# Optimization experiments

Hardware: AMD Instinct MI355X
Metric: run time of the kernel (lower is better)

The kernel has to match this reference:

```python
import jax, jax.numpy as jnp
import numpy as np

B, T, C, H = 2, 2048, 1024, 16
D = C // H  # head_dim = 64


def setup_inputs() -> dict:
    key = jax.random.key(0)
    ks = jax.random.split(key, 5)
    s = 1.0 / np.sqrt(C)
    return {
        "x": jax.random.normal(ks[0], (B, T, C), jnp.float32),
        "Wq": jax.random.normal(ks[1], (C, C), jnp.float32) * s,
        "bq": jnp.zeros((C,), jnp.float32),
        "Wk": jax.random.normal(ks[2], (C, C), jnp.float32) * s,
        "bk": jnp.zeros((C,), jnp.float32),
        "Wv": jax.random.normal(ks[3], (C, C), jnp.float32) * s,
        "bv": jnp.zeros((C,), jnp.float32),
        "Wo": jax.random.normal(ks[4], (C, C), jnp.float32) * s,
        "bo": jnp.zeros((C,), jnp.float32),
    }


def reference(x, Wq, bq, Wk, bk, Wv, bv, Wo, bo):
    Bx, Tx, Cx = x.shape
    # torch Linear: y = x @ W.T + b
    q = (x @ Wq.T + bq).reshape(Bx, Tx, H, D).transpose(0, 2, 1, 3)  # [B,H,T,D]
    k = (x @ Wk.T + bk).reshape(Bx, Tx, H, D).transpose(0, 2, 1, 3)
    v = (x @ Wv.T + bv).reshape(Bx, Tx, H, D).transpose(0, 2, 1, 3)
    att = jnp.einsum("bhqd,bhkd->bhqk", q, k) / np.sqrt(D).astype(np.float32)
    mask = jnp.tril(jnp.ones((Tx, Tx), bool))  # causal mask [T,T]
    att = jnp.where(mask, att, -jnp.inf)
    att = jax.nn.softmax(att, axis=-1)
    out = jnp.einsum("bhqk,bhkd->bhqd", att, v)
    out = out.transpose(0, 2, 1, 3).reshape(Bx, Tx, Cx)
    return out @ Wo.T + bo
```

## Files before the change

kernel.cpp:

```cpp
#include <hip/hip_runtime.h>
#include <hip/hip_bf16.h>

#define B_ 2
#define T_ 2048
#define C_ 1024
#define H_ 16
#define D_ 64

typedef unsigned short u16;
typedef __bf16 bf16x8 __attribute__((ext_vector_type(8)));
typedef float floatx4 __attribute__((ext_vector_type(4)));

__device__ __forceinline__ float bf2f(u16 u) {
  union { unsigned int i; float f; } x; x.i = ((unsigned int)u) << 16; return x.f;
}
__device__ __forceinline__ u16 f2bf(float f) {
  union { float f; unsigned int i; } x; x.f = f;
  unsigned int r = x.i + 0x7fffu + ((x.i >> 16) & 1u);
  return (u16)(r >> 16);
}

__device__ __forceinline__ unsigned cvtpk(float lo, float hi) {
  unsigned r;
  asm("v_cvt_pk_bf16_f32 %0, %1, %2" : "=v"(r) : "v"(lo), "v"(hi));
  return r;
}

__device__ __forceinline__ void gld16(void* lds, const void* g) {
  __builtin_amdgcn_global_load_lds(
      (const __attribute__((address_space(1))) unsigned int*)g,
      (__attribute__((address_space(3))) unsigned int*)lds, 16, 0, 0);
}

#define NXF4 1048576
#define NWF4 262144

__global__ __launch_bounds__(256) void cvt_all(
    const float* __restrict__ x,  const float* __restrict__ Wq,
    const float* __restrict__ Wk, const float* __restrict__ Wv,
    const float* __restrict__ Wo, u16* __restrict__ dst_base)
{
  const int i = blockIdx.x * 256 + threadIdx.x;
  const float* src; size_t off;
  if (i < NXF4)               { src = x;  off = i; }
  else if (i < NXF4 + NWF4)   { src = Wq; off = i - NXF4; }
  else if (i < NXF4 + 2*NWF4) { src = Wk; off = i - (NXF4 + NWF4); }
  else if (i < NXF4 + 3*NWF4) { src = Wv; off = i - (NXF4 + 2*NWF4); }
  else                        { src = Wo; off = i - (NXF4 + 3*NWF4); }
  float4 f = ((const float4*)src)[off];
  ushort4 o;
  o.x = f2bf(f.x); o.y = f2bf(f.y); o.z = f2bf(f.z); o.w = f2bf(f.w);
  ((ushort4*)dst_base)[i] = o;
}

#define QSCALE 0.1803368801111f

#define MFMA16(MH, NH, BREG)                                                  \
  do {                                                                        \
    __builtin_amdgcn_s_setprio(1);                                            \
    _Pragma("unroll")                                                         \
    for (int f = 0; f < 4; ++f) {                                             \
      _Pragma("unroll")                                                       \
      for (int g = 0; g < 2; ++g) {                                           \
        acc[(MH)*4 + f][(NH)*2 + g] = __builtin_amdgcn_mfma_f32_16x16x32_bf16(\
            a[f][0], BREG[g][0], acc[(MH)*4 + f][(NH)*2 + g], 0, 0, 0);       \
        acc[(MH)*4 + f][(NH)*2 + g] = __builtin_amdgcn_mfma_f32_16x16x32_bf16(\
            a[f][1], BREG[g][1], acc[(MH)*4 + f][(NH)*2 + g], 0, 0, 0);       \
      }                                                                       \
    }                                                                         \
    __builtin_amdgcn_s_setprio(0);                                            \
  } while (0)

#define PBAR()                                                \
  do {                                                        \
    asm volatile("" ::: "memory");                            \
    __builtin_amdgcn_s_barrier();                             \
    asm volatile("s_waitcnt lgkmcnt(0)" ::: "memory");        \
  } while (0)

#define EBAR()                                                \
  do {                                                        \
    asm volatile("" ::: "memory");                            \
    __builtin_amdgcn_s_barrier();                             \
    asm volatile("" ::: "memory");                            \
  } while (0)

__global__ __launch_bounds__(512, 2) void gemm_qkv8(
    const u16* __restrict__ X, const u16* __restrict__ Wb,
    const float* __restrict__ b0, const float* __restrict__ b1,
    const float* __restrict__ b2,
    u16* __restrict__ Yq, u16* __restrict__ Yk, u16* __restrict__ Yv)
{
  __shared__ __align__(16) u16 L[65536];

  const int tid  = threadIdx.x;
  const int lane = tid & 63;
  const int m16  = lane & 15;
  const int q4   = lane >> 4;
  const int wv   = tid >> 6;
  const int wm   = wv >> 2;
  const int wn   = wv & 3;

  const int bid = blockIdx.x;
  const int xcd = bid & 7;
  const int idx = bid >> 3;
  const int bx  = (xcd & 3) * 4 + (idx & 3);
  const int by  = (xcd >> 2) * 6 + (idx >> 2);

  const u16* Abase  = X  + (size_t)bx * 256 * C_;
  const u16* Bbase  = Wb + (size_t)by * 256 * C_;
  const u16* A1base = Abase + (size_t)128 * C_;
  const u16* B1base = Bbase + (size_t)128 * C_;

  const int s0 = tid,       r0 = s0 >> 3;
  const int s1 = tid + 512, r1 = s1 >> 3;
  const int k0a = ((s0 & 7) ^ (r0 & 7)) * 8;
  const int k1a = ((s1 & 7) ^ (r1 & 7)) * 8;

#define STAGE(dsthalf, srcrows, kofs)                                         \
  do {                                                                        \
    gld16(&(dsthalf)[s0 * 8], (srcrows) + (size_t)r0 * C_ + (kofs) + k0a);    \
    gld16(&(dsthalf)[s1 * 8], (srcrows) + (size_t)r1 * C_ + (kofs) + k1a);    \
  } while (0)

  u16* buf0 = L;
  u16* buf1 = L + 32768;

  STAGE(buf0 + 16384, Bbase, 0);
  STAGE(buf0,         Abase, 0);
  STAGE(buf0 + 24576, B1base, 0);
  STAGE(buf0 + 8192,  A1base, 0);
  STAGE(buf1 + 16384, Bbase, 64);
  STAGE(buf1,         Abase, 64);
  asm volatile("s_waitcnt vmcnt(4)" ::: "memory");
  __builtin_amdgcn_s_barrier();
  asm volatile("" ::: "memory");

  floatx4 acc[8][4] = {};

  const int a0off = m16 * 64 + ((q4      ^ (lane & 7)) * 8);
  const int a1off = m16 * 64 + (((q4 + 4) ^ (lane & 7)) * 8);
  const int bro   = (wn & 1) * 4096;

  for (int i = 0; i < 16; ++i) {
    u16* buf  = (i & 1) ? buf1 : buf0;
    u16* bufn = (i & 1) ? buf0 : buf1;
    const u16* Ah = buf + wm * 8192;
    const u16* Bh = buf + 16384 + (wn >> 1) * 8192;
    const bool p1 = (i + 1) < 16;
    const bool p2 = (i + 2) < 16;
    const int  k1 = (i + 1) * 64;
    const int  k2 = (i + 2) * 64;

    bf16x8 a[4][2], bA[2][2], bB[2][2];

#pragma unroll
    for (int f = 0; f < 4; ++f) {
      a[f][0] = *(const bf16x8*)&Ah[f * 1024 + a0off];
      a[f][1] = *(const bf16x8*)&Ah[f * 1024 + a1off];
    }
#pragma unroll
    for (int g = 0; g < 2; ++g) {
      bA[g][0] = *(const bf16x8*)&Bh[bro + g * 1024 + a0off];
      bA[g][1] = *(const bf16x8*)&Bh[bro + g * 1024 + a1off];
    }
    if (p1) STAGE(bufn + 24576, B1base, k1);
    PBAR();
    MFMA16(0, 0, bA);
    EBAR();

#pragma unroll
    for (int g = 0; g < 2; ++g) {
      bB[g][0] = *(const bf16x8*)&Bh[bro + 2048 + g * 1024 + a0off];
      bB[g][1] = *(const bf16x8*)&Bh[bro + 2048 + g * 1024 + a1off];
    }
    if (p1) STAGE(bufn + 8192, A1base, k1);
    PBAR();
    MFMA16(0, 1, bB);
    EBAR();

#pragma unroll
    for (int f = 0; f < 4; ++f) {
      a[f][0] = *(const bf16x8*)&Ah[4096 + f * 1024 + a0off];
      a[f][1] = *(const bf16x8*)&Ah[4096 + f * 1024 + a1off];
    }
    if (p2) STAGE(buf + 16384, Bbase, k2);
    PBAR();
    MFMA16(1, 1, bB);
    EBAR();

    if (p2) STAGE(buf, Abase, k2);
    PBAR();
    MFMA16(1, 0, bA);
    asm volatile("" ::: "memory");
    if (p2) asm volatile("s_waitcnt vmcnt(4)" ::: "memory");
    else    asm volatile("s_waitcnt vmcnt(0)" ::: "memory");
    __builtin_amdgcn_s_barrier();
    asm volatile("" ::: "memory");
  }

  const int z    = by >> 2;
  const int nloc = (by & 3) * 256 + wn * 64;
  const float* bias = (z == 0) ? b0 : (z == 1) ? b1 : b2;
  const int mbase = bx * 256 + wm * 128 + q4 * 4;

  if (z == 2) {
#pragma unroll
    for (int nf = 0; nf < 4; ++nf) {
      const int nz = nloc + nf * 16 + m16;
      const float bv = bias[nz];
      const int h = nz >> 6, d = nz & (D_ - 1);
#pragma unroll
      for (int mf = 0; mf < 8; ++mf) {
        const int m  = mbase + mf * 16;
        const int bb = m >> 11, t = m & (T_ - 1);
        ushort4 pk;
        pk.x = f2bf(acc[mf][nf][0] + bv);
        pk.y = f2bf(acc[mf][nf][1] + bv);
        pk.z = f2bf(acc[mf][nf][2] + bv);
        pk.w = f2bf(acc[mf][nf][3] + bv);
        *(ushort4*)&Yv[(((size_t)bb * H_ + h) * D_ + d) * T_ + t] = pk;
      }
    }
  } else {
    u16* Y = z ? Yk : Yq;
    const float sc = z ? 1.0f : QSCALE;
#pragma unroll
    for (int nf = 0; nf < 4; ++nf) {
      const int nz = nloc + nf * 16 + m16;
      const float bv = bias[nz];
      const int h = nz >> 6, d = nz & (D_ - 1);
#pragma unroll
      for (int mf = 0; mf < 8; ++mf) {
        const int m  = mbase + mf * 16;
        const int bb = m >> 11, tq = m & (T_ - 1);
#pragma unroll
        for (int r = 0; r < 4; ++r) {
          Y[(((size_t)bb * H_ + h) * T_ + (tq + r)) * D_ + d] =
              f2bf((acc[mf][nf][r] + bv) * sc);
        }
      }
    }
  }
}

__global__ __launch_bounds__(256) void gemm_out(
    const u16* __restrict__ X, const u16* __restrict__ W,
    const float* __restrict__ bias, float* __restrict__ Yf)
{
  const int K = C_, N = C_;
  __shared__ __align__(16) u16 As[128 * 32];
  __shared__ __align__(16) u16 Bs[64 * 32];

  const int tid  = threadIdx.x;
  const int wv   = tid >> 6;
  const int lane = tid & 63;
  const int mcol = lane & 15;
  const int quad = lane >> 4;
  const int wr = wv >> 1, wc = wv & 1;
  const int m0 = blockIdx.x * 128;
  const int n0 = blockIdx.y * 64;

  const int srow = tid >> 2;
  const int scol = (tid & 3) * 8;
  const u16* xp0 = X + (size_t)(m0 + srow) * K + scol;
  const u16* xp1 = xp0 + (size_t)64 * K;
  const u16* wp  = W + (size_t)(n0 + srow) * K + scol;

  floatx4 acc[4][2] = {};

  for (int k0 = 0; k0 < K; k0 += 32) {
    gld16(&As[tid * 8],        xp0 + k0);
    gld16(&As[2048 + tid * 8], xp1 + k0);
    gld16(&Bs[tid * 8],        wp + k0);
    __syncthreads();

    bf16x8 a[4], b[2];
#pragma unroll
    for (int rf = 0; rf < 4; ++rf)
      a[rf] = *(const bf16x8*)&As[(wr * 64 + rf * 16 + mcol) * 32 + quad * 8];
#pragma unroll
    for (int cf = 0; cf < 2; ++cf)
      b[cf] = *(const bf16x8*)&Bs[(wc * 32 + cf * 16 + mcol) * 32 + quad * 8];
#pragma unroll
    for (int rf = 0; rf < 4; ++rf)
#pragma unroll
      for (int cf = 0; cf < 2; ++cf)
        acc[rf][cf] = __builtin_amdgcn_mfma_f32_16x16x32_bf16(
            a[rf], b[cf], acc[rf][cf], 0, 0, 0);
    __syncthreads();
  }

#pragma unroll
  for (int cf = 0; cf < 2; ++cf) {
    const int n = n0 + wc * 32 + cf * 16 + mcol;
    const float bv = bias[n];
#pragma unroll
    for (int rf = 0; rf < 4; ++rf) {
#pragma unroll
      for (int r = 0; r < 4; ++r) {
        const int m = m0 + wr * 64 + rf * 16 + quad * 4 + r;
        Yf[(size_t)m * N + n] = acc[rf][cf][r] + bv;
      }
    }
  }
}

#define KSB 4096
#define VTB 5120

__global__ __launch_bounds__(256, 4) void attn_flash(
    const u16* __restrict__ Q, const u16* __restrict__ K,
    const u16* __restrict__ Vg, u16* __restrict__ O,
    float* __restrict__ OP, float* __restrict__ LP)
{
  __shared__ __align__(16) u16 Ks[2 * KSB];
  __shared__ __align__(16) u16 Vt[2 * VTB];

  const int tid  = threadIdx.x;
  const int wv   = tid >> 6;
  const int lane = tid & 63;
  const int mcol = lane & 15;
  const int quad = lane >> 4;

  const int bx = blockIdx.x;
  const int bh = bx & 31;
  const int t  = bx >> 5;
  const int iq = (t < 16) ? 31 - t : 47 - t;
  const bool pc = (t < 32);
  const int j0 = (t >= 16 && t < 32) ? 16 : 0;
  const int j1 = (t < 16) ? 15 : iq;
  const int ti = pc ? ((bh * 16 + (iq - 16)) * 2 + (j0 ? 1 : 0)) : 0;

  const size_t base  = (size_t)bh * T_ * D_;
  const size_t vbase = (size_t)bh * D_ * T_;
  const int b = bh >> 4, h = bh & (H_ - 1);

  for (int idx = tid; idx < 16 * 64; idx += 256) {
    const u16 val = (idx < 64) ? (u16)0x3F80 : (u16)0;
    Vt[64 * 64 + idx]       = val;
    Vt[VTB + 64 * 64 + idx] = val;
  }

  const int srow = lane >> 3;
  const int sg   = (lane & 7) ^ srow;
  const int c0 = wv * 2, c1 = wv * 2 + 1;
  const int sl0 = (quad ^ (mcol & 7)) * 8;

  const size_t koff0 = base + (size_t)(c0 * 8 + srow) * D_ + sg * 8;
  const size_t koff1 = base + (size_t)(c1 * 8 + srow) * D_ + sg * 8;
  const size_t voff0 = vbase + (size_t)(c0 * 8 + srow) * T_ + sg * 8;
  const size_t voff1 = vbase + (size_t)(c1 * 8 + srow) * T_ + sg * 8;

  const u16* qg = Q + base + (size_t)(iq * 64 + wv * 16 + mcol) * D_ + quad * 8;
  const bf16x8 qf0 = *(const bf16x8*)qg;
  const bf16x8 qf1 = *(const bf16x8*)(qg + 32);

  floatx4 oacc[5] = {};

  __syncthreads();
  {
    const size_t kj = (size_t)j0 * 64 * D_;
    const int    vj = j0 * 64;
    gld16(&Ks[c0 * 512 + lane * 8], K  + koff0 + kj);
    gld16(&Ks[c1 * 512 + lane * 8], K  + koff1 + kj);
    gld16(&Vt[c0 * 512 + lane * 8], Vg + voff0 + vj);
    gld16(&Vt[c1 * 512 + lane * 8], Vg + voff1 + vj);
  }

  for (int j = j0; j <= j1; ++j) {
    const int cur = (j - j0) & 1;
    __syncthreads();

    if (j < j1) {
      const int nb = cur ^ 1;
      const size_t kj = (size_t)(j + 1) * 64 * D_;
      const int    vj = (j + 1) * 64;
      gld16(&Ks[nb * KSB + c0 * 512 + lane * 8], K  + koff0 + kj);
      gld16(&Ks[nb * KSB + c1 * 512 + lane * 8], K  + koff1 + kj);
      gld16(&Vt[nb * VTB + c0 * 512 + lane * 8], Vg + voff0 + vj);
      gld16(&Vt[nb * VTB + c1 * 512 + lane * 8], Vg + voff1 + vj);
    }

    const u16* ksb = &Ks[cur * KSB];
    const u16* vtb = &Vt[cur * VTB];

    floatx4 sacc[4] = {};
#pragma unroll
    for (int nt = 0; nt < 4; ++nt) {
      const u16* kr = &ksb[(nt * 16 + mcol) * 64];
      bf16x8 kb0 = *(const bf16x8*)&kr[sl0];
      bf16x8 kb1 = *(const bf16x8*)&kr[sl0 ^ 32];
      sacc[nt] = __builtin_amdgcn_mfma_f32_16x16x32_bf16(kb0, qf0, sacc[nt], 0, 0, 0);
      sacc[nt] = __builtin_amdgcn_mfma_f32_16x16x32_bf16(kb1, qf1, sacc[nt], 0, 0, 0);
    }

    if (j == iq) {
      const int ql = wv * 16 + mcol;
#pragma unroll
      for (int nt = 0; nt < 4; ++nt) {
#pragma unroll
        for (int r = 0; r < 4; ++r)
          if (nt * 16 + quad * 4 + r > ql) sacc[nt][r] = -1e30f;
      }
    }

    unsigned w0[2], w1[2], w2[2], w3[2];
#pragma unroll
    for (int i = 0; i < 2; ++i) {
      w0[i] = cvtpk(exp2f(sacc[0][2*i]), exp2f(sacc[0][2*i+1]));
      w1[i] = cvtpk(exp2f(sacc[1][2*i]), exp2f(sacc[1][2*i+1]));
      w2[i] = cvtpk(exp2f(sacc[2][2*i]), exp2f(sacc[2][2*i+1]));
      w3[i] = cvtpk(exp2f(sacc[3][2*i]), exp2f(sacc[3][2*i+1]));
    }

    union { unsigned u[4]; bf16x8 v; } pa0u, pa1u;
#pragma unroll
    for (int i = 0; i < 2; ++i) {
      unsigned x = w0[i], y = w1[i];
      asm("v_permlane32_swap_b32 %0, %1" : "+v"(x), "+v"(y));
      asm("v_permlane16_swap_b32 %0, %1" : "+v"(x), "+v"(y));
      pa0u.u[i] = x; pa0u.u[i + 2] = y;
      unsigned x2 = w2[i], y2 = w3[i];
      asm("v_permlane32_swap_b32 %0, %1" : "+v"(x2), "+v"(y2));
      asm("v_permlane16_swap_b32 %0, %1" : "+v"(x2), "+v"(y2));
      pa1u.u[i] = x2; pa1u.u[i + 2] = y2;
    }
    const bf16x8 pa0 = pa0u.v;
    const bf16x8 pa1 = pa1u.v;

#pragma unroll
    for (int dt = 0; dt < 5; ++dt) {
      const u16* vr = &vtb[(dt * 16 + mcol) * 64];
      bf16x8 vb0 = *(const bf16x8*)&vr[sl0];
      bf16x8 vb1 = *(const bf16x8*)&vr[sl0 ^ 32];
      oacc[dt] = __builtin_amdgcn_mfma_f32_16x16x32_bf16(pa0, vb0, oacc[dt], 0, 0, 0);
      oacc[dt] = __builtin_amdgcn_mfma_f32_16x16x32_bf16(pa1, vb1, oacc[dt], 0, 0, 0);
    }
  }

  if (!pc) {
    float invl[4];
#pragma unroll
    for (int r = 0; r < 4; ++r)
      invl[r] = 1.f / __shfl(oacc[4][r], lane & 48);
#pragma unroll
    for (int dt = 0; dt < 4; ++dt) {
      const int c = h * D_ + dt * 16 + mcol;
#pragma unroll
      for (int r = 0; r < 4; ++r) {
        const int tg = iq * 64 + wv * 16 + quad * 4 + r;
        O[((size_t)b * T_ + tg) * C_ + c] = f2bf(oacc[dt][r] * invl[r]);
      }
    }
  } else {
    float* op = OP + (size_t)ti * 4096;
#pragma unroll
    for (int dt = 0; dt < 4; ++dt)
#pragma unroll
      for (int r = 0; r < 4; ++r)
        op[(wv * 16 + quad * 4 + r) * 64 + dt * 16 + mcol] = oacc[dt][r];
    if (mcol == 0) {
#pragma unroll
      for (int r = 0; r < 4; ++r)
        LP[ti * 64 + wv * 16 + quad * 4 + r] = oacc[4][r];
    }
  }
}

__global__ __launch_bounds__(256) void attn_merge(
    const float* __restrict__ OP, const float* __restrict__ LP,
    u16* __restrict__ O)
{
  const int mb = blockIdx.x;
  const int bh = mb & 31, qt = mb >> 5;
  const int iq = 16 + qt;
  const int ti0 = (bh * 16 + qt) * 2;
  const int b = bh >> 4, h = bh & (H_ - 1);
  const int row = threadIdx.x >> 2;
  const int dc  = (threadIdx.x & 3) * 16;

  const float l = LP[ti0 * 64 + row] + LP[(ti0 + 1) * 64 + row];
  const float inv = 1.f / l;
  const float* pa = OP + (size_t)ti0 * 4096 + row * 64 + dc;
  const float* pb = pa + 4096;

  const int tg = iq * 64 + row;
  u16* o = O + ((size_t)b * T_ + tg) * C_ + h * D_ + dc;

  u16 tmp[16];
#pragma unroll
  for (int i = 0; i < 4; ++i) {
    const float4 a4 = ((const float4*)pa)[i];
    const float4 b4 = ((const float4*)pb)[i];
    tmp[i*4 + 0] = f2bf((a4.x + b4.x) * inv);
    tmp[i*4 + 1] = f2bf((a4.y + b4.y) * inv);
    tmp[i*4 + 2] = f2bf((a4.z + b4.z) * inv);
    tmp[i*4 + 3] = f2bf((a4.w + b4.w) * inv);
  }
  *(uint4*)&o[0] = *(const uint4*)&tmp[0];
  *(uint4*)&o[8] = *(const uint4*)&tmp[8];
}

extern "C" void kernel_launch(void* const* d_in, const int* in_sizes, int n_in,
                              void* d_out, int out_size, void* d_ws, size_t ws_size,
                              hipStream_t stream) {
  const float* x  = (const float*)d_in[0];
  const float* Wq = (const float*)d_in[1];
  const float* bq = (const float*)d_in[2];
  const float* Wk = (const float*)d_in[3];
  const float* bk = (const float*)d_in[4];
  const float* Wv = (const float*)d_in[5];
  const float* bv = (const float*)d_in[6];
  const float* Wo = (const float*)d_in[7];
  const float* bo = (const float*)d_in[8];
  float* out = (float*)d_out;

  const size_t NX = (size_t)B_ * T_ * C_;
  const size_t NW = (size_t)C_ * C_;

  u16* xb  = (u16*)d_ws;
  u16* wqb = xb  + NX;
  u16* wkb = wqb + NW;
  u16* wvb = wkb + NW;
  u16* wob = wvb + NW;
  u16* q   = wob + NW;
  u16* k   = q   + NX;
  u16* v   = k   + NX;
  u16* ctx = v   + NX;
  float* opart = (float*)(ctx + NX);
  float* lpart = opart + (size_t)1024 * 4096;

  cvt_all<<<dim3((NXF4 + 4 * NWF4) / 256), 256, 0, stream>>>(x, Wq, Wk, Wv, Wo, xb);

  gemm_qkv8<<<dim3(192), 512, 0, stream>>>(xb, wqb, bq, bk, bv, q, k, v);

  attn_flash<<<dim3(1536), 256, 0, stream>>>(q, k, v, ctx, opart, lpart);

  attn_merge<<<dim3(512), 256, 0, stream>>>(opart, lpart, ctx);

  gemm_out<<<dim3(32, 16), 256, 0, stream>>>(ctx, wob, bo, out);
}
```

Before: 183.9 us.

## Retile QKV GEMM to 256x192 tiles so 256 blocks fill all CUs

Result: no change. 181.5 us (-1.3%).

```diff
diff --git a/kernel.cpp b/kernel.cpp
--- a/kernel.cpp
+++ b/kernel.cpp
@@ -55,22 +55,6 @@
 
 #define QSCALE 0.1803368801111f
 
-#define MFMA16(MH, NH, BREG)                                                  \
-  do {                                                                        \
-    __builtin_amdgcn_s_setprio(1);                                            \
-    _Pragma("unroll")                                                         \
-    for (int f = 0; f < 4; ++f) {                                             \
-      _Pragma("unroll")                                                       \
-      for (int g = 0; g < 2; ++g) {                                           \
-        acc[(MH)*4 + f][(NH)*2 + g] = __builtin_amdgcn_mfma_f32_16x16x32_bf16(\
-            a[f][0], BREG[g][0], acc[(MH)*4 + f][(NH)*2 + g], 0, 0, 0);       \
-        acc[(MH)*4 + f][(NH)*2 + g] = __builtin_amdgcn_mfma_f32_16x16x32_bf16(\
-            a[f][1], BREG[g][1], acc[(MH)*4 + f][(NH)*2 + g], 0, 0, 0);       \
-      }                                                                       \
-    }                                                                         \
-    __builtin_amdgcn_s_setprio(0);                                            \
-  } while (0)
-
 #define PBAR()                                                \
   do {                                                        \
     asm volatile("" ::: "memory");                            \
@@ -91,7 +75,7 @@
     const float* __restrict__ b2,
     u16* __restrict__ Yq, u16* __restrict__ Yk, u16* __restrict__ Yv)
 {
-  __shared__ __align__(16) u16 L[65536];
+  __shared__ __align__(16) u16 L[57344];
 
   const int tid  = threadIdx.x;
   const int lane = tid & 63;
@@ -105,54 +89,59 @@
   const int xcd = bid & 7;
   const int idx = bid >> 3;
   const int bx  = (xcd & 3) * 4 + (idx & 3);
-  const int by  = (xcd >> 2) * 6 + (idx >> 2);
+  const int by  = (xcd >> 2) * 8 + (idx >> 2);
 
   const u16* Abase  = X  + (size_t)bx * 256 * C_;
-  const u16* Bbase  = Wb + (size_t)by * 256 * C_;
+  const u16* Bbase  = Wb + (size_t)by * 192 * C_;
   const u16* A1base = Abase + (size_t)128 * C_;
-  const u16* B1base = Bbase + (size_t)128 * C_;
-
-  const int s0 = tid,       r0 = s0 >> 3;
-  const int s1 = tid + 512, r1 = s1 >> 3;
-  const int k0a = ((s0 & 7) ^ (r0 & 7)) * 8;
-  const int k1a = ((s1 & 7) ^ (r1 & 7)) * 8;
-
-#define STAGE(dsthalf, srcrows, kofs)                                         \
+
+  const int rB  = tid >> 3;
+  const int s0 = tid,       r0 = rB;
+  const int s1 = tid + 512, r1 = 64 + rB;
+  const int k0a = ((tid & 7) ^ (rB & 7)) * 8;
+
+#define STAGE_A(dsthalf, srcrows, kofs)                                       \
   do {                                                                        \
     gld16(&(dsthalf)[s0 * 8], (srcrows) + (size_t)r0 * C_ + (kofs) + k0a);    \
-    gld16(&(dsthalf)[s1 * 8], (srcrows) + (size_t)r1 * C_ + (kofs) + k1a);    \
+    gld16(&(dsthalf)[s1 * 8], (srcrows) + (size_t)r1 * C_ + (kofs) + k0a);    \
   } while (0)
 
+#define STAGE_BL(dstB, srcrows, kofs, l)                                      \
+  gld16(&(dstB)[((l) * 512 + tid) * 8],                                       \
+        (srcrows) + (size_t)((l) * 64 + rB) * C_ + (kofs) + k0a)
+
   u16* buf0 = L;
-  u16* buf1 = L + 32768;
-
-  STAGE(buf0 + 16384, Bbase, 0);
-  STAGE(buf0,         Abase, 0);
-  STAGE(buf0 + 24576, B1base, 0);
-  STAGE(buf0 + 8192,  A1base, 0);
-  STAGE(buf1 + 16384, Bbase, 64);
-  STAGE(buf1,         Abase, 64);
+  u16* buf1 = L + 28672;
+
+  STAGE_BL(buf0 + 16384, Bbase, 0, 0);
+  STAGE_BL(buf0 + 16384, Bbase, 0, 1);
+  STAGE_BL(buf0 + 16384, Bbase, 0, 2);
+  STAGE_A (buf0,         Abase,  0);
+  STAGE_A (buf0 + 8192,  A1base, 0);
+  STAGE_BL(buf1 + 16384, Bbase, 64, 0);
+  STAGE_BL(buf1 + 16384, Bbase, 64, 1);
+  STAGE_A (buf1,         Abase, 64);
   asm volatile("s_waitcnt vmcnt(4)" ::: "memory");
   __builtin_amdgcn_s_barrier();
   asm volatile("" ::: "memory");
 
-  floatx4 acc[8][4] = {};
+  floatx4 acc[8][3] = {};
 
   const int a0off = m16 * 64 + ((q4      ^ (lane & 7)) * 8);
   const int a1off = m16 * 64 + (((q4 + 4) ^ (lane & 7)) * 8);
-  const int bro   = (wn & 1) * 4096;
+  const int bro   = wn * 3072;
 
   for (int i = 0; i < 16; ++i) {
     u16* buf  = (i & 1) ? buf1 : buf0;
     u16* bufn = (i & 1) ? buf0 : buf1;
     const u16* Ah = buf + wm * 8192;
-    const u16* Bh = buf + 16384 + (wn >> 1) * 8192;
+    const u16* Bh = buf + 16384;
     const bool p1 = (i + 1) < 16;
     const bool p2 = (i + 2) < 16;
     const int  k1 = (i + 1) * 64;
     const int  k2 = (i + 2) * 64;
 
-    bf16x8 a[4][2], bA[2][2], bB[2][2];
+    bf16x8 a[4][2], bA[2][2], bB[2];
 
 #pragma unroll
     for (int f = 0; f < 4; ++f) {
@@ -164,19 +153,30 @@
       bA[g][0] = *(const bf16x8*)&Bh[bro + g * 1024 + a0off];
       bA[g][1] = *(const bf16x8*)&Bh[bro + g * 1024 + a1off];
     }
-    if (p1) STAGE(bufn + 24576, B1base, k1);
+    if (p1) STAGE_A(bufn + 8192, A1base, k1);
     PBAR();
-    MFMA16(0, 0, bA);
+    __builtin_amdgcn_s_setprio(1);
+#pragma unroll
+    for (int f = 0; f < 4; ++f)
+#pragma unroll
+      for (int g = 0; g < 2; ++g) {
+        acc[f][g] = __builtin_amdgcn_mfma_f32_16x16x32_bf16(a[f][0], bA[g][0], acc[f][g], 0, 0, 0);
+        acc[f][g] = __builtin_amdgcn_mfma_f32_16x16x32_bf16(a[f][1], bA[g][1], acc[f][g], 0, 0, 0);
+      }
+    __builtin_amdgcn_s_setprio(0);
     EBAR();
 
-#pragma unroll
-    for (int g = 0; g < 2; ++g) {
-      bB[g][0] = *(const bf16x8*)&Bh[bro + 2048 + g * 1024 + a0off];
-      bB[g][1] = *(const bf16x8*)&Bh[bro + 2048 + g * 1024 + a1off];
-    }
-    if (p1) STAGE(bufn + 8192, A1base, k1);
+    bB[0] = *(const bf16x8*)&Bh[bro + 2048 + a0off];
+    bB[1] = *(const bf16x8*)&Bh[bro + 2048 + a1off];
+    if (p1) STAGE_BL(bufn + 16384, Bbase, k1, 2);
     PBAR();
-    MFMA16(0, 1, bB);
+    __builtin_amdgcn_s_setprio(1);
+#pragma unroll
+    for (int f = 0; f < 4; ++f) {
+      acc[f][2] = __builtin_amdgcn_mfma_f32_16x16x32_bf16(a[f][0], bB[0], acc[f][2], 0, 0, 0);
+      acc[f][2] = __builtin_amdgcn_mfma_f32_16x16x32_bf16(a[f][1], bB[1], acc[f][2], 0, 0, 0);
+    }
+    __builtin_amdgcn_s_setprio(0);
     EBAR();
 
 #pragma unroll
@@ -184,14 +184,31 @@
       a[f][0] = *(const bf16x8*)&Ah[4096 + f * 1024 + a0off];
       a[f][1] = *(const bf16x8*)&Ah[4096 + f * 1024 + a1off];
     }
-    if (p2) STAGE(buf + 16384, Bbase, k2);
+    if (p2) {
+      STAGE_BL(buf + 16384, Bbase, k2, 0);
+      STAGE_BL(buf + 16384, Bbase, k2, 1);
+    }
     PBAR();
-    MFMA16(1, 1, bB);
+    __builtin_amdgcn_s_setprio(1);
+#pragma unroll
+    for (int f = 0; f < 4; ++f) {
+      acc[4 + f][2] = __builtin_amdgcn_mfma_f32_16x16x32_bf16(a[f][0], bB[0], acc[4 + f][2], 0, 0, 0);
+      acc[4 + f][2] = __builtin_amdgcn_mfma_f32_16x16x32_bf16(a[f][1], bB[1], acc[4 + f][2], 0, 0, 0);
+    }
+    __builtin_amdgcn_s_setprio(0);
     EBAR();
 
-    if (p2) STAGE(buf, Abase, k2);
+    if (p2) STAGE_A(buf, Abase, k2);
     PBAR();
-    MFMA16(1, 0, bA);
+    __builtin_amdgcn_s_setprio(1);
+#pragma unroll
+    for (int f = 0; f < 4; ++f)
+#pragma unroll
+      for (int g = 0; g < 2; ++g) {
+        acc[4 + f][g] = __builtin_amdgcn_mfma_f32_16x16x32_bf16(a[f][0], bA[g][0], acc[4 + f][g], 0, 0, 0);
+        acc[4 + f][g] = __builtin_amdgcn_mfma_f32_16x16x32_bf16(a[f][1], bA[g][1], acc[4 + f][g], 0, 0, 0);
+      }
+    __builtin_amdgcn_s_setprio(0);
     asm volatile("" ::: "memory");
     if (p2) asm volatile("s_waitcnt vmcnt(4)" ::: "memory");
     else    asm volatile("s_waitcnt vmcnt(0)" ::: "memory");
@@ -199,17 +216,15 @@
     asm volatile("" ::: "memory");
   }
 
-  const int z    = by >> 2;
-  const int nloc = (by & 3) * 256 + wn * 64;
-  const float* bias = (z == 0) ? b0 : (z == 1) ? b1 : b2;
   const int mbase = bx * 256 + wm * 128 + q4 * 4;
-
-  if (z == 2) {
-#pragma unroll
-    for (int nf = 0; nf < 4; ++nf) {
-      const int nz = nloc + nf * 16 + m16;
-      const float bv = bias[nz];
-      const int h = nz >> 6, d = nz & (D_ - 1);
+#pragma unroll
+  for (int nf = 0; nf < 3; ++nf) {
+    const int nzg = by * 192 + wn * 48 + nf * 16 + m16;
+    const int z  = nzg >> 10;
+    const int nl = nzg & 1023;
+    const int h = nl >> 6, d = nl & (D_ - 1);
+    const float bv = (z == 0 ? b0 : z == 1 ? b1 : b2)[nl];
+    if (z == 2) {
 #pragma unroll
       for (int mf = 0; mf < 8; ++mf) {
         const int m  = mbase + mf * 16;
@@ -221,15 +236,9 @@
         pk.w = f2bf(acc[mf][nf][3] + bv);
         *(ushort4*)&Yv[(((size_t)bb * H_ + h) * D_ + d) * T_ + t] = pk;
       }
-    }
-  } else {
-    u16* Y = z ? Yk : Yq;
-    const float sc = z ? 1.0f : QSCALE;
-#pragma unroll
-    for (int nf = 0; nf < 4; ++nf) {
-      const int nz = nloc + nf * 16 + m16;
-      const float bv = bias[nz];
-      const int h = nz >> 6, d = nz & (D_ - 1);
+    } else {
+      u16* Y = z ? Yk : Yq;
+      const float sc = z ? 1.0f : QSCALE;
 #pragma unroll
       for (int mf = 0; mf < 8; ++mf) {
         const int m  = mbase + mf * 16;
@@ -533,7 +542,7 @@
 
   cvt_all<<<dim3((NXF4 + 4 * NWF4) / 256), 256, 0, stream>>>(x, Wq, Wk, Wv, Wo, xb);
 
-  gemm_qkv8<<<dim3(192), 512, 0, stream>>>(xb, wqb, bq, bk, bv, q, k, v);
+  gemm_qkv8<<<dim3(256), 512, 0, stream>>>(xb, wqb, bq, bk, bv, q, k, v);
 
   attn_flash<<<dim3(1536), 256, 0, stream>>>(q, k, v, ctx, opart, lpart);
 
```
